# Kernel tuning notes

Hardware: AMD Instinct MI355X
Metric: run time of the kernel (lower is better)

## Reference

```python
import jax, jax.numpy as jnp
import numpy as np

D_MODEL = 1024
N_HEAD = 16


def setup_inputs() -> dict:
    key = jax.random.key(0)
    k1, k2, k3 = jax.random.split(key, 3)
    scale = 1.0 / np.sqrt(D_MODEL)
    x = jax.random.normal(k1, (1, 4096, D_MODEL), dtype=jnp.float32)
    # nn.Linear weights stored as [out, in]; applied as x @ W.T
    w_attn = jax.random.normal(k2, (3 * D_MODEL, D_MODEL), dtype=jnp.float32) * scale
    w_proj = jax.random.normal(k3, (D_MODEL, D_MODEL), dtype=jnp.float32) * scale
    return {"x": x, "w_attn": w_attn, "w_proj": w_proj}


def reference(x, w_attn, w_proj):
    B, T, C = x.shape
    H = N_HEAD
    hd = C // H
    qkv = x @ w_attn.T                      # [B, T, 3C]
    q, k, v = jnp.split(qkv, 3, axis=-1)
    # [B, T, C] -> [B, H, T, hd]
    q = q.reshape(B, T, H, hd).transpose(0, 2, 1, 3)
    k = k.reshape(B, T, H, hd).transpose(0, 2, 1, 3)
    v = v.reshape(B, T, H, hd).transpose(0, 2, 1, 3)
    att = jnp.einsum("bhqd,bhkd->bhqk", q, k) * (1.0 / np.sqrt(hd))  # [B,H,T,T]
    causal = jnp.tril(jnp.ones((T, T), dtype=bool))
    att = jnp.where(causal[None, None], att, -jnp.inf)
    att = jax.nn.softmax(att, axis=-1)
    y = jnp.einsum("bhqk,bhkd->bhqd", att, v)  # [B,H,T,hd]
    y = y.transpose(0, 2, 1, 3).reshape(B, T, C)
    return y @ w_proj.T
```

## Files before the change

kernel.cpp:

```cpp
#include <hip/hip_runtime.h>
#include <hip/hip_bf16.h>
#include <stdint.h>

typedef __bf16 bf16x8 __attribute__((ext_vector_type(8)));
typedef float f32x4 __attribute__((ext_vector_type(4)));

#define T_SEQ 4096
#define C_DIM 1024
#define H_NUM 16
#define HD 64
#define C3 3072
#define NEG_BIG (-30000.0f)

__device__ __forceinline__ unsigned short f2bf(float f) {
    uint32_t u = __builtin_bit_cast(uint32_t, f);
    u += 0x7fffu + ((u >> 16) & 1u);
    return (unsigned short)(u >> 16);
}

__device__ __forceinline__ uint32_t pk_bf16(float a, float b) {
    __hip_bfloat162 h = __float22bfloat162_rn(float2{a, b});
    uint32_t u;
    __builtin_memcpy(&u, &h, sizeof(u));
    return u;
}

__device__ __forceinline__ bf16x8 ld_bf8(const unsigned short* p) {
    return *reinterpret_cast<const bf16x8*>(p);
}

__device__ __forceinline__ void async_g2l16(const unsigned short* g, unsigned short* l) {
    __builtin_amdgcn_global_load_lds(
        (const __attribute__((address_space(1))) void*)g,
        (__attribute__((address_space(3))) void*)l, 16, 0, 0);
}

__device__ __forceinline__ void store_c(unsigned short* C, size_t idx, float v) { C[idx] = f2bf(v); }
__device__ __forceinline__ void store_c(float* C, size_t idx, float v)          { C[idx] = v; }

__device__ __forceinline__ void cvt8(const float* src, unsigned short* dst) {
    float4 f0 = *(const float4*)src;
    float4 f1 = *(const float4*)(src + 4);
    union { uint32_t w[4]; uint4 q; } t;
    t.w[0] = pk_bf16(f0.x, f0.y);
    t.w[1] = pk_bf16(f0.z, f0.w);
    t.w[2] = pk_bf16(f1.x, f1.y);
    t.w[3] = pk_bf16(f1.z, f1.w);
    *(uint4*)dst = t.q;
}

__global__ void cvt_all(const float* __restrict__ x, const float* __restrict__ wa,
                        const float* __restrict__ wp,
                        unsigned short* __restrict__ xb, unsigned short* __restrict__ wab,
                        unsigned short* __restrict__ wpb) {
    int i = (blockIdx.x * blockDim.x + threadIdx.x) * 8;
    if (i < T_SEQ * C_DIM) { cvt8(x + i, xb + i); return; }
    i -= T_SEQ * C_DIM;
    if (i < C3 * C_DIM) { cvt8(wa + i, wab + i); return; }
    i -= C3 * C_DIM;
    if (wpb != nullptr && i < C_DIM * C_DIM) cvt8(wp + i, wpb + i);
}

__global__ void cvt_f32_bf16(const float* __restrict__ src, unsigned short* __restrict__ dst, int n) {
    int i = (blockIdx.x * blockDim.x + threadIdx.x) * 8;
    if (i >= n) return;
    cvt8(src + i, dst + i);
}

template <int BM, typename TC>
__global__ __launch_bounds__(BM * 2, (BM == 128) ? 2 : 3) void gemm_bt(
    const unsigned short* __restrict__ A, const unsigned short* __restrict__ B,
    TC* __restrict__ C, unsigned short* __restrict__ VT, int M, int N, int K)
{
    __shared__ __attribute__((aligned(16))) unsigned short As[BM * 32];
    __shared__ __attribute__((aligned(16))) unsigned short Bs[128 * 32];

    const int tid  = threadIdx.x;
    const int wave = tid >> 6, lane = tid & 63;
    const int quad = lane >> 4, l16 = lane & 15;
    const int wm = (BM == 128) ? (wave >> 1) : 0;
    const int wn = (BM == 128) ? (wave & 1) : wave;
    const int m0 = blockIdx.y * BM, n0 = blockIdx.x * 128;

    const int sr   = lane >> 2;
    const int scol = (lane & 3) * 8;

    f32x4 acc[4][4] = {};

    for (int k0 = 0; k0 < K; k0 += 32) {
        if constexpr (BM == 128) {
            const unsigned short* ga = A + (size_t)(m0 + wave * 32 + sr) * K + k0 + scol;
            const unsigned short* gb = B + (size_t)(n0 + wave * 32 + sr) * K + k0 + scol;
            unsigned short* la = As + (wave * 32) * 32;
            unsigned short* lb = Bs + (wave * 32) * 32;
            async_g2l16(ga, la);
            async_g2l16(ga + (size_t)16 * K, la + 16 * 32);
            async_g2l16(gb, lb);
            async_g2l16(gb + (size_t)16 * K, lb + 16 * 32);
        } else {
            const unsigned short* ga = A + (size_t)(m0 + wave * 32 + sr) * K + k0 + scol;
            unsigned short* la = As + (wave * 32) * 32;
            async_g2l16(ga, la);
            async_g2l16(ga + (size_t)16 * K, la + 16 * 32);
            const unsigned short* gb = B + (size_t)(n0 + wave * 64 + sr) * K + k0 + scol;
            unsigned short* lb = Bs + (wave * 64) * 32;
            async_g2l16(gb, lb);
            async_g2l16(gb + (size_t)16 * K, lb + 16 * 32);
            async_g2l16(gb + (size_t)32 * K, lb + 32 * 32);
            async_g2l16(gb + (size_t)48 * K, lb + 48 * 32);
        }
        __syncthreads();

        bf16x8 af[4], bf[4];
        #pragma unroll
        for (int i = 0; i < 4; ++i) {
            af[i] = ld_bf8(As + (wm * 64 + i * 16 + l16) * 32 + quad * 8);
            bf[i] = ld_bf8(Bs + (wn * 64 + i * 16 + l16) * 32 + quad * 8);
        }
        #pragma unroll
        for (int mt = 0; mt < 4; ++mt)
            #pragma unroll
            for (int nt = 0; nt < 4; ++nt)
                acc[mt][nt] = __builtin_amdgcn_mfma_f32_16x16x32_bf16(
                    af[mt], bf[nt], acc[mt][nt], 0, 0, 0);
        __syncthreads();
    }

    if (VT != nullptr && n0 >= 2 * C_DIM) {
        #pragma unroll
        for (int mt = 0; mt < 4; ++mt)
            #pragma unroll
            for (int nt = 0; nt < 4; ++nt) {
                const int ch = n0 - 2 * C_DIM + wn * 64 + nt * 16 + l16;
                const int t0 = m0 + wm * 64 + mt * 16 + quad * 4;
                union { unsigned short u[4]; uint2 q; } pk;
                #pragma unroll
                for (int r = 0; r < 4; ++r) pk.u[r] = f2bf(acc[mt][nt][r]);
                *(uint2*)(VT + (size_t)ch * T_SEQ + t0) = pk.q;
            }
    } else {
        #pragma unroll
        for (int mt = 0; mt < 4; ++mt)
            #pragma unroll
            for (int nt = 0; nt < 4; ++nt)
                #pragma unroll
                for (int r = 0; r < 4; ++r) {
                    int row = m0 + wm * 64 + mt * 16 + quad * 4 + r;
                    int col = n0 + wn * 64 + nt * 16 + l16;
                    store_c(C, (size_t)row * N + col, acc[mt][nt][r]);
                }
    }
}

#if __has_builtin(__builtin_amdgcn_permlane32_swap) && __has_builtin(__builtin_amdgcn_permlane16_swap)
#define HAVE_PERMLANE_SWAP 1
#else
#define HAVE_PERMLANE_SWAP 0
#endif

__device__ __forceinline__ void quad_xpose_pair(uint32_t X, uint32_t Y,
                                                uint32_t& t0, uint32_t& t1) {
#if HAVE_PERMLANE_SWAP
    auto S = __builtin_amdgcn_permlane32_swap((int)X, (int)Y, false, false);
    auto T = __builtin_amdgcn_permlane16_swap((int)S[0], (int)S[1], false, false);
    t0 = (uint32_t)T[0];
    t1 = (uint32_t)T[1];
#else
    const unsigned l = threadIdx.x & 63;
    uint32_t Ys = (uint32_t)__shfl_xor((int)Y, 32, 64);
    uint32_t Xs = (uint32_t)__shfl_xor((int)X, 32, 64);
    uint32_t S0 = (l < 32) ? X : Ys;
    uint32_t S1 = (l < 32) ? Xs : Y;
    uint32_t S0s = (uint32_t)__shfl_xor((int)S0, 16, 64);
    uint32_t S1s = (uint32_t)__shfl_xor((int)S1, 16, 64);
    t0 = (l & 16) ? S1s : S0;
    t1 = (l & 16) ? S1 : S0s;
#endif
}

template <bool MASK>
__device__ __forceinline__ void fa7_tile(
    const unsigned short* Ksb, const unsigned short* Vsb,
    const bf16x8 qf[2][2], f32x4 o[2][4], float* l_part,
    int k0, int q_abs0, int quad, int l16, int fo0, int fo1)
{
    const unsigned short* krow = Ksb + l16 * 64;
    bf16x8 kf[4][2];
    #pragma unroll
    for (int s = 0; s < 4; ++s) {
        kf[s][0] = ld_bf8(krow + s * 1024 + fo0);
        kf[s][1] = ld_bf8(krow + s * 1024 + fo1);
    }

    bf16x8 pf[2][2];
    #pragma unroll
    for (int qs = 0; qs < 2; ++qs) {
        f32x4 st[4];
        __builtin_amdgcn_s_setprio(1);
        #pragma unroll
        for (int s = 0; s < 4; ++s) {
            f32x4 z = {};
            z = __builtin_amdgcn_mfma_f32_16x16x32_bf16(kf[s][0], qf[qs][0], z, 0, 0, 0);
            st[s] = __builtin_amdgcn_mfma_f32_16x16x32_bf16(kf[s][1], qf[qs][1], z, 0, 0, 0);
        }
        __builtin_amdgcn_s_setprio(0);

        float ts = 0.f;
        #pragma unroll
        for (int s = 0; s < 4; ++s)
            #pragma unroll
            for (int r = 0; r < 4; ++r) {
                float v = st[s][r];
                if (MASK) {
                    int key = k0 + s * 16 + quad * 4 + r;
                    v = (key <= q_abs0 + qs * 16) ? v : NEG_BIG;
                }
                float e = __builtin_amdgcn_exp2f(v);
                st[s][r] = e;
                ts += e;
            }
        l_part[qs] += ts;

        uint32_t W[4][2];
        #pragma unroll
        for (int s = 0; s < 4; ++s) {
            W[s][0] = pk_bf16(st[s][0], st[s][1]);
            W[s][1] = pk_bf16(st[s][2], st[s][3]);
        }
        union { uint32_t w[4]; bf16x8 v; } pA, pB;
        quad_xpose_pair(W[0][0], W[1][0], pA.w[0], pA.w[2]);
        quad_xpose_pair(W[0][1], W[1][1], pA.w[1], pA.w[3]);
        quad_xpose_pair(W[2][0], W[3][0], pB.w[0], pB.w[2]);
        quad_xpose_pair(W[2][1], W[3][1], pB.w[1], pB.w[3]);
        pf[qs][0] = pA.v;
        pf[qs][1] = pB.v;
    }

    const unsigned short* vrow = Vsb + l16 * 64;
    bf16x8 vf[4][2];
    #pragma unroll
    for (int c = 0; c < 4; ++c) {
        vf[c][0] = ld_bf8(vrow + c * 1024 + fo0);
        vf[c][1] = ld_bf8(vrow + c * 1024 + fo1);
    }
    __builtin_amdgcn_s_setprio(1);
    #pragma unroll
    for (int qs = 0; qs < 2; ++qs)
        #pragma unroll
        for (int c = 0; c < 4; ++c) {
            o[qs][c] = __builtin_amdgcn_mfma_f32_16x16x32_bf16(vf[c][0], pf[qs][0], o[qs][c], 0, 0, 0);
            o[qs][c] = __builtin_amdgcn_mfma_f32_16x16x32_bf16(vf[c][1], pf[qs][1], o[qs][c], 0, 0, 0);
        }
    __builtin_amdgcn_s_setprio(0);
}

__global__ __launch_bounds__(256, 2) void flash_attn8(
    const unsigned short* __restrict__ qkv,
    const unsigned short* __restrict__ Vt,
    unsigned short* __restrict__ Y)
{
    __shared__ __attribute__((aligned(16))) unsigned short Ks[2][2][4096];
    __shared__ __attribute__((aligned(16))) unsigned short Vs[2][2][4096];

    const int tid  = threadIdx.x;
    const int wave = tid >> 6, lane = tid & 63;
    const int quad = lane >> 4, l16 = lane & 15;
    const int wq = wave >> 1, wk = wave & 1;

    const int bi = blockIdx.x;
    const int h  = bi & 15;
    const int qb = (bi < 512) ? (63 - (bi >> 4)) : (31 - ((bi - 512) >> 4));

    const int q0w    = qb * 64 + wq * 32;
    const int q_abs0 = q0w + l16;
    const int sw  = l16 & 7;
    const int fo0 = (quad ^ sw) * 8;
    const int fo1 = ((quad + 4) ^ sw) * 8;

    bf16x8 qf[2][2];
    {
        const float QS = 0.125f * 1.44269504f;
        #pragma unroll
        for (int qs = 0; qs < 2; ++qs) {
            const unsigned short* qp =
                qkv + (size_t)(q0w + qs * 16 + l16) * C3 + h * HD + quad * 8;
            bf16x8 a = ld_bf8(qp), b = ld_bf8(qp + 32);
            #pragma unroll
            for (int i = 0; i < 8; ++i) {
                qf[qs][0][i] = (__bf16)((float)a[i] * QS);
                qf[qs][1][i] = (__bf16)((float)b[i] * QS);
            }
        }
    }

    const int srow   = lane >> 3;
    const int schunk = (lane & 7) ^ srow;
    const unsigned short* kp =
        qkv + (size_t)(wq * 64 + wk * 32 + srow) * C3 + C_DIM + h * HD + schunk * 8;
    const unsigned short* vp =
        Vt + (size_t)(h * HD + wk * 32 + srow) * T_SEQ + wq * 64 + schunk * 8;
    unsigned short* lk = &Ks[0][wq][(wk * 32) * 64];
    unsigned short* lv = &Vs[0][wq][(wk * 32) * 64];
    const int lds_db = 2 * 4096;
    const size_t kstep = (size_t)8 * C3;
    const size_t vstep = (size_t)8 * T_SEQ;

    auto stage = [&](int b) {
        #pragma unroll
        for (int jj = 0; jj < 4; ++jj) {
            async_g2l16(kp + jj * kstep, lk + b * lds_db + jj * 8 * 64);
            async_g2l16(vp + jj * vstep, lv + b * lds_db + jj * 8 * 64);
        }
    };

    f32x4 o[2][4] = {};
    float l_part[2] = {0.f, 0.f};

    const int nt = qb + 1;
    const int R  = (nt + 1) >> 1;
    stage(0);
    kp += (size_t)128 * C3; vp += 128;

    for (int r = 0; r < R; ++r) {
        __syncthreads();
        const int b = r & 1;
        if (r + 1 < R) {
            stage(1 - b);
            kp += (size_t)128 * C3; vp += 128;
        }
        const int t = 2 * r + wk;
        if (t < nt) {
            if (t == nt - 1)
                fa7_tile<true>(&Ks[b][wk][0], &Vs[b][wk][0], qf, o, l_part,
                               t * 64, q_abs0, quad, l16, fo0, fo1);
            else
                fa7_tile<false>(&Ks[b][wk][0], &Vs[b][wk][0], qf, o, l_part,
                                t * 64, q_abs0, quad, l16, fo0, fo1);
        }
    }

    __syncthreads();
    float* red  = (float*)&Ks[0][0][0];
    float* lred = (float*)&Vs[0][0][0];
    if (wk == 1) {
        #pragma unroll
        for (int qs = 0; qs < 2; ++qs)
            #pragma unroll
            for (int c = 0; c < 4; ++c)
                *(f32x4*)&red[((wq * 8 + qs * 4 + c) * 64 + lane) * 4] = o[qs][c];
        lred[wq * 128 + lane * 2 + 0] = l_part[0];
        lred[wq * 128 + lane * 2 + 1] = l_part[1];
    }
    __syncthreads();
    if (wk == 0) {
        #pragma unroll
        for (int qs = 0; qs < 2; ++qs) {
            #pragma unroll
            for (int c = 0; c < 4; ++c) {
                f32x4 p = *(f32x4*)&red[((wq * 8 + qs * 4 + c) * 64 + lane) * 4];
                o[qs][c] += p;
            }
            l_part[qs] += lred[wq * 128 + lane * 2 + qs];
        }

        #pragma unroll
        for (int qs = 0; qs < 2; ++qs) {
            float l = l_part[qs];
            l += __shfl_xor(l, 16, 64);
            l += __shfl_xor(l, 32, 64);
            float inv_l = 1.f / l;
            #pragma unroll
            for (int c = 0; c < 4; ++c) {
                union { uint32_t w[2]; uint2 q; } t;
                t.w[0] = pk_bf16(o[qs][c][0] * inv_l, o[qs][c][1] * inv_l);
                t.w[1] = pk_bf16(o[qs][c][2] * inv_l, o[qs][c][3] * inv_l);
                *(uint2*)(Y + (size_t)(q_abs0 + qs * 16) * C_DIM + h * HD + c * 16 + quad * 4) = t.q;
            }
        }
    }
}

extern "C" void kernel_launch(void* const* d_in, const int* in_sizes, int n_in,
                              void* d_out, int out_size, void* d_ws, size_t ws_size,
                              hipStream_t stream) {
    const float* x      = (const float*)d_in[0];
    const float* w_attn = (const float*)d_in[1];
    const float* w_proj = (const float*)d_in[2];
    float* out = (float*)d_out;

    unsigned short* qkv = (unsigned short*)d_ws;
    unsigned short* xb  = qkv + (size_t)T_SEQ * C3;
    unsigned short* y   = xb;
    unsigned short* Vt  = (unsigned short*)d_out;
    unsigned short* wab = Vt + (size_t)C_DIM * T_SEQ;

    const size_t need = ((size_t)T_SEQ * C3 + (size_t)T_SEQ * C_DIM +
                         (size_t)C_DIM * C_DIM) * sizeof(unsigned short);
    const bool fuse_wp = ws_size >= need;
    unsigned short* wpb = fuse_wp ? (xb + (size_t)T_SEQ * C_DIM)
                                  : qkv;

    if (fuse_wp) {
        const int n8 = (T_SEQ * C_DIM + C3 * C_DIM + C_DIM * C_DIM) / 8;
        cvt_all<<<n8 / 256, 256, 0, stream>>>(x, w_attn, w_proj, xb, wab, wpb);
    } else {
        const int n8 = (T_SEQ * C_DIM + C3 * C_DIM) / 8;
        cvt_all<<<n8 / 256, 256, 0, stream>>>(x, w_attn, nullptr, xb, wab, nullptr);
    }

    gemm_bt<128, unsigned short>
        <<<dim3(C3 / 128, T_SEQ / 128), 256, 0, stream>>>(xb, wab, qkv, Vt, T_SEQ, C3, C_DIM);

    flash_attn8<<<dim3(1024), 256, 0, stream>>>(qkv, Vt, y);

    if (!fuse_wp) {
        cvt_f32_bf16<<<(C_DIM * C_DIM / 8 + 255) / 256, 256, 0, stream>>>(w_proj, wpb, C_DIM * C_DIM);
    }

    gemm_bt<64, float>
        <<<dim3(C_DIM / 128, T_SEQ / 64), 128, 0, stream>>>(y, wpb, out, nullptr, T_SEQ, C_DIM, C_DIM);
}
```

Before: 195.3 us.

## Process 128 query rows per attention block with 8 waves sharing K/V tiles

The flash-attention kernel now launches 512 blocks of 512 threads, each covering 128 query rows instead of 64, so every staged K/V tile in LDS is reused by twice as many query waves. Loading is split so half the waves fetch K and half fetch V, and the causal mask is applied per wave based on its own query range. Blocks are ordered so long-causal work runs first to balance load. The tighter launch bounds and a larger epilogue reduction footprint may raise register pressure or limit occupancy.

```diff
diff --git a/kernel.cpp b/kernel.cpp
--- a/kernel.cpp
+++ b/kernel.cpp
@@ -254,7 +254,7 @@
     __builtin_amdgcn_s_setprio(0);
 }
 
-__global__ __launch_bounds__(256, 2) void flash_attn8(
+__global__ __launch_bounds__(512, 4) void flash_attn11(
     const unsigned short* __restrict__ qkv,
     const unsigned short* __restrict__ Vt,
     unsigned short* __restrict__ Y)
@@ -267,11 +267,13 @@
     const int quad = lane >> 4, l16 = lane & 15;
     const int wq = wave >> 1, wk = wave & 1;
 
-    const int bi = blockIdx.x;
-    const int h  = bi & 15;
-    const int qb = (bi < 512) ? (63 - (bi >> 4)) : (31 - ((bi - 512) >> 4));
-
-    const int q0w    = qb * 64 + wq * 32;
+    const int bi  = blockIdx.x;
+    const int gen = bi >> 8, s = bi & 255;
+    const int h   = s & 15;
+    const int idx = s >> 4;
+    const int j   = (gen == 0) ? (31 - idx) : idx;
+
+    const int q0w    = j * 128 + wq * 32;
     const int q_abs0 = q0w + l16;
     const int sw  = l16 & 7;
     const int fo0 = (quad ^ sw) * 8;
@@ -293,49 +295,55 @@
         }
     }
 
+    const int tt = wave >> 1, hf = wave & 1;
     const int srow   = lane >> 3;
     const int schunk = (lane & 7) ^ srow;
-    const unsigned short* kp =
-        qkv + (size_t)(wq * 64 + wk * 32 + srow) * C3 + C_DIM + h * HD + schunk * 8;
-    const unsigned short* vp =
-        Vt + (size_t)(h * HD + wk * 32 + srow) * T_SEQ + wq * 64 + schunk * 8;
-    unsigned short* lk = &Ks[0][wq][(wk * 32) * 64];
-    unsigned short* lv = &Vs[0][wq][(wk * 32) * 64];
+    const unsigned short* gp;
+    size_t gstep, rstep;
+    unsigned short* lbase;
+    if (tt < 2) {
+        gp = qkv + (size_t)(tt * 64 + hf * 32 + srow) * C3 + C_DIM + h * HD + schunk * 8;
+        gstep = (size_t)8 * C3;
+        rstep = (size_t)128 * C3;
+        lbase = &Ks[0][tt][(hf * 32) * 64];
+    } else {
+        const int vt = tt - 2;
+        gp = Vt + (size_t)(h * HD + hf * 32 + srow) * T_SEQ + vt * 64 + schunk * 8;
+        gstep = (size_t)8 * T_SEQ;
+        rstep = (size_t)128;
+        lbase = &Vs[0][vt][(hf * 32) * 64];
+    }
     const int lds_db = 2 * 4096;
-    const size_t kstep = (size_t)8 * C3;
-    const size_t vstep = (size_t)8 * T_SEQ;
 
     auto stage = [&](int b) {
         #pragma unroll
-        for (int jj = 0; jj < 4; ++jj) {
-            async_g2l16(kp + jj * kstep, lk + b * lds_db + jj * 8 * 64);
-            async_g2l16(vp + jj * vstep, lv + b * lds_db + jj * 8 * 64);
-        }
+        for (int jj = 0; jj < 4; ++jj)
+            async_g2l16(gp + jj * gstep, lbase + b * lds_db + jj * 8 * 64);
     };
 
     f32x4 o[2][4] = {};
     float l_part[2] = {0.f, 0.f};
 
-    const int nt = qb + 1;
-    const int R  = (nt + 1) >> 1;
+    const int nt = 2 * (j + 1);
+    const int R  = j + 1;
     stage(0);
-    kp += (size_t)128 * C3; vp += 128;
+    gp += rstep;
 
     for (int r = 0; r < R; ++r) {
         __syncthreads();
         const int b = r & 1;
         if (r + 1 < R) {
             stage(1 - b);
-            kp += (size_t)128 * C3; vp += 128;
+            gp += rstep;
         }
         const int t = 2 * r + wk;
-        if (t < nt) {
-            if (t == nt - 1)
+        if (t < nt && t * 64 <= q0w + 31) {
+            if (t * 64 + 63 <= q0w)
+                fa7_tile<false>(&Ks[b][wk][0], &Vs[b][wk][0], qf, o, l_part,
+                                t * 64, q_abs0, quad, l16, fo0, fo1);
+            else
                 fa7_tile<true>(&Ks[b][wk][0], &Vs[b][wk][0], qf, o, l_part,
                                t * 64, q_abs0, quad, l16, fo0, fo1);
-            else
-                fa7_tile<false>(&Ks[b][wk][0], &Vs[b][wk][0], qf, o, l_part,
-                                t * 64, q_abs0, quad, l16, fo0, fo1);
         }
     }
 
@@ -411,7 +419,7 @@
     gemm_bt<128, unsigned short>
         <<<dim3(C3 / 128, T_SEQ / 128), 256, 0, stream>>>(xb, wab, qkv, Vt, T_SEQ, C3, C_DIM);
 
-    flash_attn8<<<dim3(1024), 256, 0, stream>>>(qkv, Vt, y);
+    flash_attn11<<<dim3(512), 512, 0, stream>>>(qkv, Vt, y);
 
     if (!fuse_wp) {
         cvt_f32_bf16<<<(C_DIM * C_DIM / 8 + 255) / 256, 256, 0, stream>>>(w_proj, wpb, C_DIM * C_DIM);
```

Result: slower. 236.4 us (+21.0%).
